# Kernel tuning notes

Hardware: AMD Instinct MI355X
Metric: run time of the kernel (lower is better)

Reference implementation:

```python
import jax, jax.numpy as jnp
import numpy as np

B, S, D = 4, 1568, 1024
H = 16
HD = D // H  # 64


def setup_inputs() -> dict:
    key = jax.random.key(0)
    ks = jax.random.split(key, 9)
    scale = 0.02
    return {
        "hidden_states": jax.random.normal(ks[0], (B, S, D), dtype=jnp.float32),
        "Wq": jax.random.normal(ks[1], (D, D), dtype=jnp.float32) * scale,
        "bq": jnp.zeros((D,), dtype=jnp.float32),
        "Wk": jax.random.normal(ks[2], (D, D), dtype=jnp.float32) * scale,
        "bk": jnp.zeros((D,), dtype=jnp.float32),
        "Wv": jax.random.normal(ks[3], (D, D), dtype=jnp.float32) * scale,
        "bv": jnp.zeros((D,), dtype=jnp.float32),
        "Wp": jax.random.normal(ks[4], (D, D), dtype=jnp.float32) * scale,
        "bp": jnp.zeros((D,), dtype=jnp.float32),
    }


def reference(hidden_states, Wq, bq, Wk, bk, Wv, bv, Wp, bp):
    x = hidden_states  # [B, S, D]
    # Linear projections (torch Linear: x @ W.T + b)
    q = x @ Wq.T + bq
    k = x @ Wk.T + bk
    v = x @ Wv.T + bv
    # split heads: [B, H, S, HD]
    def heads(t):
        return t.reshape(B, S, H, HD).transpose(0, 2, 1, 3)
    q, k, v = heads(q), heads(k), heads(v)
    scale = 1.0 / jnp.sqrt(jnp.asarray(HD, dtype=q.dtype))
    scores = jnp.einsum('bhqd,bhkd->bhqk', q, k) * scale  # [B,H,S,S]
    probs = jax.nn.softmax(scores, axis=-1)
    ctx = jnp.einsum('bhqk,bhkd->bhqd', probs, v)  # [B,H,S,HD]
    ctx = ctx.transpose(0, 2, 1, 3).reshape(B, S, D)
    out = ctx @ Wp.T + bp
    return out
```

## Files before the change

kernel.cpp:

```cpp
#include <hip/hip_runtime.h>
#include <stdint.h>

#define SEQ 1568
#define SEQV 1600
#define DIM 1024
#define NB 4
#define NH 16
#define HD 64

typedef unsigned short u16;
typedef __bf16 bf16x8 __attribute__((ext_vector_type(8)));
typedef float f32x4 __attribute__((ext_vector_type(4)));

#define QSCALE 0.18033688011112042f

#define PSTR 72

__device__ __forceinline__ void load_lds16(const u16* g, u16* s) {
  __builtin_amdgcn_global_load_lds((__attribute__((address_space(1))) void*)g,
                                   (__attribute__((address_space(3))) void*)s,
                                   16, 0, 0);
}

#define WAIT_VM(N) asm volatile("s_waitcnt vmcnt(" #N ")" ::: "memory")
#define LGKM0()    asm volatile("s_waitcnt lgkmcnt(0)" ::: "memory")
#define BAR()      do { __builtin_amdgcn_s_barrier(); \
                        __builtin_amdgcn_sched_barrier(0); } while (0)

__global__ __launch_bounds__(256) void cvt_all(
    const float* __restrict__ x,  const float* __restrict__ wq,
    const float* __restrict__ wk, const float* __restrict__ wv,
    const float* __restrict__ wp,
    u16* __restrict__ xb, u16* __restrict__ wqb, u16* __restrict__ wkb,
    u16* __restrict__ wvb, u16* __restrict__ wpb) {
  int i = blockIdx.x * 256 + threadIdx.x;
  const float* src; u16* dst; int off;
  if (i < 1605632)      { src = x;  dst = xb;  off = i; }
  else if (i < 1867776) { src = wq; dst = wqb; off = i - 1605632; }
  else if (i < 2129920) { src = wk; dst = wkb; off = i - 1867776; }
  else if (i < 2392064) { src = wv; dst = wvb; off = i - 2129920; }
  else                  { src = wp; dst = wpb; off = i - 2392064; }
  float4 v = ((const float4*)src)[off];
  union { unsigned long long u; __bf16 h[4]; } o;
  o.h[0] = (__bf16)v.x; o.h[1] = (__bf16)v.y;
  o.h[2] = (__bf16)v.z; o.h[3] = (__bf16)v.w;
  ((unsigned long long*)dst)[off] = o.u;
}

__global__ __launch_bounds__(256) void gemm_qkv(
    const u16* __restrict__ xb,
    const u16* __restrict__ wq, const u16* __restrict__ wk, const u16* __restrict__ wv,
    const float* __restrict__ bq, const float* __restrict__ bk, const float* __restrict__ bv,
    u16* __restrict__ qo, u16* __restrict__ ko, u16* __restrict__ vto) {
  const int bid = blockIdx.x + (blockIdx.y << 3) + blockIdx.z * 416;
  const int logical = (bid & 7) * 156 + (bid >> 3);
  const int byz = logical >> 3;
  const int by  = byz % 52;
  const int z   = byz / 52;
  const int bi  = by / 13;
  const int st  = by % 13;
  const int bn  = (logical & 7) * 128;

  const u16* W = (z == 0) ? wq : (z == 1) ? wk : wv;
  const float* bias = (z == 0) ? bq : (z == 1) ? bk : bv;

  __shared__ __align__(16) u16 sA[3][128 * 32];
  __shared__ __align__(16) u16 sB[3][128 * 32];

  const int tid = threadIdx.x;
  const int wave = tid >> 6;
  const int lane = tid & 63;
  const int l15 = lane & 15;
  const int quad = lane >> 4;
  const int wm = (wave >> 1) * 64;
  const int wn = (wave & 1) * 64;

  const int sr  = lane >> 2;
  const int scs = (((lane & 3) ^ ((lane >> 3) & 3)) << 3);
  const int r0 = wave * 32;

  int ra1 = st * 128 + r0 + sr;       if (ra1 >= SEQ) ra1 = SEQ - 1;
  int ra2 = st * 128 + r0 + 16 + sr;  if (ra2 >= SEQ) ra2 = SEQ - 1;
  const u16* gA1 = xb + (size_t)(bi * SEQ + ra1) * DIM + scs;
  const u16* gA2 = xb + (size_t)(bi * SEQ + ra2) * DIM + scs;
  const u16* gB1 = W + (size_t)(bn + r0 + sr) * DIM + scs;
  const u16* gB2 = gB1 + 16 * DIM;

  f32x4 acc[4][4] = {};
  const int rsw = (l15 >> 1) & 3;

  auto stage = [&](int kk, u16* sAc, u16* sBc) {
    load_lds16(gA1 + kk, sAc + r0 * 32);
    load_lds16(gA2 + kk, sAc + (r0 + 16) * 32);
    load_lds16(gB1 + kk, sBc + r0 * 32);
    load_lds16(gB2 + kk, sBc + (r0 + 16) * 32);
  };

  auto mstep = [&](const u16* sAc, const u16* sBc) {
    bf16x8 a[4], b[4];
#pragma unroll
    for (int mt = 0; mt < 4; mt++)
      a[mt] = *(const bf16x8*)&sAc[(wm + mt * 16 + l15) * 32 + ((quad ^ rsw) << 3)];
#pragma unroll
    for (int nt = 0; nt < 4; nt++)
      b[nt] = *(const bf16x8*)&sBc[(wn + nt * 16 + l15) * 32 + ((quad ^ rsw) << 3)];
#pragma unroll
    for (int mt = 0; mt < 4; mt++)
#pragma unroll
      for (int nt = 0; nt < 4; nt++)
        acc[mt][nt] = __builtin_amdgcn_mfma_f32_16x16x32_bf16(a[mt], b[nt], acc[mt][nt], 0, 0, 0);
  };

  stage(0,  &sA[0][0], &sB[0][0]);
  stage(32, &sA[1][0], &sB[1][0]);
  stage(64, &sA[2][0], &sB[2][0]);

#pragma unroll 1
  for (int t = 0; t < 30; t += 3) {
    WAIT_VM(8); BAR();
    mstep(&sA[0][0], &sB[0][0]);
    LGKM0(); BAR();
    stage((t + 3) * 32, &sA[0][0], &sB[0][0]);

    WAIT_VM(8); BAR();
    mstep(&sA[1][0], &sB[1][0]);
    LGKM0(); BAR();
    stage((t + 4) * 32, &sA[1][0], &sB[1][0]);

    WAIT_VM(8); BAR();
    mstep(&sA[2][0], &sB[2][0]);
    LGKM0(); BAR();
    if (t + 5 < 32) stage((t + 5) * 32, &sA[2][0], &sB[2][0]);
  }
  WAIT_VM(4); BAR();
  mstep(&sA[0][0], &sB[0][0]);
  WAIT_VM(0); BAR();
  mstep(&sA[1][0], &sB[1][0]);

#pragma unroll
  for (int nt = 0; nt < 4; nt++) {
    const int n = bn + wn + nt * 16 + l15;
    const float bia = bias[n];
    const int h = n >> 6, d = n & 63;
#pragma unroll
    for (int mt = 0; mt < 4; mt++) {
      const int sbase = st * 128 + wm + mt * 16 + quad * 4;
#pragma unroll
      for (int r = 0; r < 4; r++) {
        const int s = sbase + r;
        if (s < SEQ) {
          float val = acc[mt][nt][r] + bia;
          if (z == 0) val *= QSCALE;
          const __bf16 o = (__bf16)val;
          if (z == 0)
            *(__bf16*)&qo[(((size_t)(bi * NH + h)) * SEQ + s) * HD + d] = o;
          else if (z == 1)
            *(__bf16*)&ko[(((size_t)(bi * NH + h)) * SEQ + s) * HD + d] = o;
          else
            *(__bf16*)&vto[(((size_t)(bi * NH + h)) * HD + d) * SEQV + s] = o;
        }
      }
    }
  }
}

__global__ __launch_bounds__(256, 4) void attn(
    const u16* __restrict__ q, const u16* __restrict__ k,
    const u16* __restrict__ vt, u16* __restrict__ ctx) {
  const int bh = blockIdx.y;
  const int qt = blockIdx.x;
  const int tid = threadIdx.x;
  const int wave = tid >> 6, lane = tid & 63, l15 = lane & 15, quad = lane >> 4;

  __shared__ __align__(16) u16 sK[64 * 64];
  __shared__ __align__(16) u16 sV[64 * 64];
  __shared__ __align__(16) u16 sP[4][32 * PSTR];

  const u16* qh = q + (size_t)bh * (SEQ * HD);
  const u16* kh = k + (size_t)bh * (SEQ * HD);
  const u16* vh = vt + (size_t)bh * (HD * SEQV);

  bf16x8 aq[2][2];
#pragma unroll
  for (int mt = 0; mt < 2; mt++) {
    int qrow = qt * 128 + wave * 32 + mt * 16 + l15;
    int qr = qrow < SEQ ? qrow : SEQ - 1;
    aq[mt][0] = *(const bf16x8*)&qh[(size_t)qr * HD + quad * 8];
    aq[mt][1] = *(const bf16x8*)&qh[(size_t)qr * HD + 32 + quad * 8];
  }

  f32x4 o[2][4] = {};
  float lrow[2][4] = {};

  const int jrow = lane >> 3;
  const int cg = (lane & 7) ^ jrow;
  u16* sPw = sP[wave];
  const int j7 = l15 & 7;

  for (int j0 = 0; j0 < 1536; j0 += 64) {
    __syncthreads();
    load_lds16(&kh[(size_t)(j0 + wave * 16 + jrow) * HD + cg * 8], &sK[(wave * 16) * 64]);
    load_lds16(&kh[(size_t)(j0 + wave * 16 + 8 + jrow) * HD + cg * 8], &sK[(wave * 16 + 8) * 64]);
    load_lds16(&vh[(size_t)(wave * 16 + jrow) * SEQV + j0 + cg * 8], &sV[(wave * 16) * 64]);
    load_lds16(&vh[(size_t)(wave * 16 + 8 + jrow) * SEQV + j0 + cg * 8], &sV[(wave * 16 + 8) * 64]);
    __syncthreads();

#pragma unroll
    for (int mt = 0; mt < 2; mt++) {
      f32x4 s[4];
#pragma unroll
      for (int jt = 0; jt < 4; jt++) {
        const int j = jt * 16 + l15;
        bf16x8 b0 = *(const bf16x8*)&sK[j * 64 + ((quad ^ j7) * 8)];
        bf16x8 b1 = *(const bf16x8*)&sK[j * 64 + (((4 + quad) ^ j7) * 8)];
        f32x4 acc = {};
        acc = __builtin_amdgcn_mfma_f32_16x16x32_bf16(aq[mt][0], b0, acc, 0, 0, 0);
        acc = __builtin_amdgcn_mfma_f32_16x16x32_bf16(aq[mt][1], b1, acc, 0, 0, 0);
        s[jt] = acc;
      }
#pragma unroll
      for (int jt = 0; jt < 4; jt++)
#pragma unroll
        for (int r = 0; r < 4; r++) {
          float p = __builtin_exp2f(s[jt][r]);
          lrow[mt][r] += p;
          *(__bf16*)&sPw[(mt * 16 + quad * 4 + r) * PSTR + jt * 16 + l15] = (__bf16)p;
        }
    }

    asm volatile("s_waitcnt lgkmcnt(0)" ::: "memory");

#pragma unroll
    for (int kc = 0; kc < 2; kc++) {
      bf16x8 ap0 = *(const bf16x8*)&sPw[l15 * PSTR + kc * 32 + quad * 8];
      bf16x8 ap1 = *(const bf16x8*)&sPw[(16 + l15) * PSTR + kc * 32 + quad * 8];
#pragma unroll
      for (int dt = 0; dt < 4; dt++) {
        const int d7 = l15 & 7;
        bf16x8 bv = *(const bf16x8*)&sV[(dt * 16 + l15) * 64 + (((kc * 4 + quad) ^ d7) * 8)];
        o[0][dt] = __builtin_amdgcn_mfma_f32_16x16x32_bf16(ap0, bv, o[0][dt], 0, 0, 0);
        o[1][dt] = __builtin_amdgcn_mfma_f32_16x16x32_bf16(ap1, bv, o[1][dt], 0, 0, 0);
      }
    }
  }

  {
    const int j0 = 1536;
    __syncthreads();
    if (wave < 2) {
      load_lds16(&kh[(size_t)(j0 + wave * 16 + jrow) * HD + cg * 8], &sK[(wave * 16) * 64]);
      load_lds16(&kh[(size_t)(j0 + wave * 16 + 8 + jrow) * HD + cg * 8], &sK[(wave * 16 + 8) * 64]);
    }
    load_lds16(&vh[(size_t)(wave * 16 + jrow) * SEQV + j0 + cg * 8], &sV[(wave * 16) * 64]);
    load_lds16(&vh[(size_t)(wave * 16 + 8 + jrow) * SEQV + j0 + cg * 8], &sV[(wave * 16 + 8) * 64]);
    __syncthreads();

#pragma unroll
    for (int mt = 0; mt < 2; mt++) {
      f32x4 s[2];
#pragma unroll
      for (int jt = 0; jt < 2; jt++) {
        const int j = jt * 16 + l15;
        bf16x8 b0 = *(const bf16x8*)&sK[j * 64 + ((quad ^ j7) * 8)];
        bf16x8 b1 = *(const bf16x8*)&sK[j * 64 + (((4 + quad) ^ j7) * 8)];
        f32x4 acc = {};
        acc = __builtin_amdgcn_mfma_f32_16x16x32_bf16(aq[mt][0], b0, acc, 0, 0, 0);
        acc = __builtin_amdgcn_mfma_f32_16x16x32_bf16(aq[mt][1], b1, acc, 0, 0, 0);
        s[jt] = acc;
      }
#pragma unroll
      for (int jt = 0; jt < 2; jt++)
#pragma unroll
        for (int r = 0; r < 4; r++) {
          float p = __builtin_exp2f(s[jt][r]);
          lrow[mt][r] += p;
          *(__bf16*)&sPw[(mt * 16 + quad * 4 + r) * PSTR + jt * 16 + l15] = (__bf16)p;
        }
    }

    asm volatile("s_waitcnt lgkmcnt(0)" ::: "memory");

    {
      bf16x8 ap0 = *(const bf16x8*)&sPw[l15 * PSTR + quad * 8];
      bf16x8 ap1 = *(const bf16x8*)&sPw[(16 + l15) * PSTR + quad * 8];
#pragma unroll
      for (int dt = 0; dt < 4; dt++) {
        const int d7 = l15 & 7;
        bf16x8 bv = *(const bf16x8*)&sV[(dt * 16 + l15) * 64 + ((quad ^ d7) * 8)];
        o[0][dt] = __builtin_amdgcn_mfma_f32_16x16x32_bf16(ap0, bv, o[0][dt], 0, 0, 0);
        o[1][dt] = __builtin_amdgcn_mfma_f32_16x16x32_bf16(ap1, bv, o[1][dt], 0, 0, 0);
      }
    }
  }

  const int bi = bh >> 4, h = bh & 15;
#pragma unroll
  for (int mt = 0; mt < 2; mt++) {
#pragma unroll
    for (int r = 0; r < 4; r++) {
      float l = lrow[mt][r];
#pragma unroll
      for (int off = 8; off >= 1; off >>= 1) l += __shfl_xor(l, off, 16);
      const int srow = qt * 128 + wave * 32 + mt * 16 + quad * 4 + r;
      if (srow < SEQ) {
        const float inv = 1.0f / l;
#pragma unroll
        for (int dt = 0; dt < 4; dt++)
          *(__bf16*)&ctx[((size_t)(bi * SEQ + srow)) * DIM + h * HD + dt * 16 + l15] =
              (__bf16)(o[mt][dt][r] * inv);
      }
    }
  }
}

__global__ __launch_bounds__(256) void gemm_out(
    const u16* __restrict__ ctx, const u16* __restrict__ wp,
    const float* __restrict__ bp, float* __restrict__ out) {
  __shared__ __align__(16) u16 sA[128 * 32];
  __shared__ __align__(16) u16 sB[128 * 32];

  const int tid = threadIdx.x;
  const int wave = tid >> 6;
  const int lane = tid & 63;
  const int l15 = lane & 15;
  const int quad = lane >> 4;
  const int bm = blockIdx.y * 128;
  const int bn = blockIdx.x * 128;
  const int wm = (wave >> 1) * 64;
  const int wn = (wave & 1) * 64;
  const int sr = lane >> 2;
  const int sc = (lane & 3) * 8;
  const int r0 = wave * 32;

  f32x4 acc[4][4] = {};

  for (int k0 = 0; k0 < DIM; k0 += 32) {
    __syncthreads();
    {
      const u16* gA = ctx + (size_t)(bm + r0 + sr) * DIM + k0 + sc;
      load_lds16(gA, &sA[r0 * 32]);
      load_lds16(gA + 16 * DIM, &sA[(r0 + 16) * 32]);
      const u16* gB = wp + (size_t)(bn + r0 + sr) * DIM + k0 + sc;
      load_lds16(gB, &sB[r0 * 32]);
      load_lds16(gB + 16 * DIM, &sB[(r0 + 16) * 32]);
    }
    __syncthreads();

    bf16x8 a[4], b[4];
#pragma unroll
    for (int mt = 0; mt < 4; mt++)
      a[mt] = *(const bf16x8*)&sA[(wm + mt * 16 + l15) * 32 + quad * 8];
#pragma unroll
    for (int nt = 0; nt < 4; nt++)
      b[nt] = *(const bf16x8*)&sB[(wn + nt * 16 + l15) * 32 + quad * 8];
#pragma unroll
    for (int mt = 0; mt < 4; mt++)
#pragma unroll
      for (int nt = 0; nt < 4; nt++)
        acc[mt][nt] = __builtin_amdgcn_mfma_f32_16x16x32_bf16(a[mt], b[nt], acc[mt][nt], 0, 0, 0);
  }

#pragma unroll
  for (int nt = 0; nt < 4; nt++) {
    const int n = bn + wn + nt * 16 + l15;
    const float bia = bp[n];
#pragma unroll
    for (int mt = 0; mt < 4; mt++) {
      const int mbase = bm + wm + mt * 16 + quad * 4;
#pragma unroll
      for (int r = 0; r < 4; r++)
        out[(size_t)(mbase + r) * DIM + n] = acc[mt][nt][r] + bia;
    }
  }
}

extern "C" void kernel_launch(void* const* d_in, const int* in_sizes, int n_in,
                              void* d_out, int out_size, void* d_ws, size_t ws_size,
                              hipStream_t stream) {
  const float* x  = (const float*)d_in[0];
  const float* Wq = (const float*)d_in[1];
  const float* bq = (const float*)d_in[2];
  const float* Wk = (const float*)d_in[3];
  const float* bk = (const float*)d_in[4];
  const float* Wv = (const float*)d_in[5];
  const float* bv = (const float*)d_in[6];
  const float* Wp = (const float*)d_in[7];
  const float* bp = (const float*)d_in[8];
  float* out = (float*)d_out;

  char* ws = (char*)d_ws;
  u16* xb   = (u16*)(ws + 0);
  u16* wqb  = (u16*)(ws + 12845056);
  u16* wkb  = (u16*)(ws + 14942208);
  u16* wvb  = (u16*)(ws + 17039360);
  u16* wpb  = (u16*)(ws + 19136512);
  u16* qb   = (u16*)(ws + 21233664);
  u16* kb   = (u16*)(ws + 34078720);
  u16* vtb  = (u16*)(ws + 46923776);
  u16* ctxb = (u16*)(ws + 60030976);

  cvt_all<<<10368, 256, 0, stream>>>(x, Wq, Wk, Wv, Wp, xb, wqb, wkb, wvb, wpb);
  gemm_qkv<<<dim3(8, 52, 3), 256, 0, stream>>>(xb, wqb, wkb, wvb, bq, bk, bv, qb, kb, vtb);
  attn<<<dim3(13, 64), 256, 0, stream>>>(qb, kb, vtb, ctxb);
  gemm_out<<<dim3(8, 49), 256, 0, stream>>>(ctxb, wpb, bp, out);
}
```

Baseline: 295.6 us.

## Transpose S MFMA operands for packed P stores and remap attention blocks

The QK^T MFMA operands are swapped so each lane holds a score column per query row. Each lane can then pack four bf16 probabilities into one 8-byte LDS store instead of four scalar 2-byte stores, and keep a single running row sum per tile. The row-sum reduction becomes two cross-quad shuffles plus a broadcast. The grid is flattened to 1D with a remap that interleaves blocks by groups of 8 (likely to spread each head's K/V reuse across XCDs/L2), at the cost of a little integer div/mod per block.

Result: no change. 291.8 us (-1.3%).

```diff
diff --git a/kernel.cpp b/kernel.cpp
--- a/kernel.cpp
+++ b/kernel.cpp
@@ -10,6 +10,7 @@
 
 typedef unsigned short u16;
 typedef __bf16 bf16x8 __attribute__((ext_vector_type(8)));
+typedef __bf16 bf16x4 __attribute__((ext_vector_type(4)));
 typedef float f32x4 __attribute__((ext_vector_type(4)));
 
 #define QSCALE 0.18033688011112042f
@@ -167,8 +168,10 @@
 __global__ __launch_bounds__(256, 4) void attn(
     const u16* __restrict__ q, const u16* __restrict__ k,
     const u16* __restrict__ vt, u16* __restrict__ ctx) {
-  const int bh = blockIdx.y;
-  const int qt = blockIdx.x;
+  const int bid = blockIdx.x;
+  const int logical = (bid & 7) * 104 + (bid >> 3);
+  const int bh = logical / 13;
+  const int qt = logical % 13;
   const int tid = threadIdx.x;
   const int wave = tid >> 6, lane = tid & 63, l15 = lane & 15, quad = lane >> 4;
 
@@ -190,7 +193,7 @@
   }
 
   f32x4 o[2][4] = {};
-  float lrow[2][4] = {};
+  float lsum[2] = {0.0f, 0.0f};
 
   const int jrow = lane >> 3;
   const int cg = (lane & 7) ^ jrow;
@@ -214,21 +217,24 @@
         bf16x8 b0 = *(const bf16x8*)&sK[j * 64 + ((quad ^ j7) * 8)];
         bf16x8 b1 = *(const bf16x8*)&sK[j * 64 + (((4 + quad) ^ j7) * 8)];
         f32x4 acc = {};
-        acc = __builtin_amdgcn_mfma_f32_16x16x32_bf16(aq[mt][0], b0, acc, 0, 0, 0);
-        acc = __builtin_amdgcn_mfma_f32_16x16x32_bf16(aq[mt][1], b1, acc, 0, 0, 0);
+        acc = __builtin_amdgcn_mfma_f32_16x16x32_bf16(b0, aq[mt][0], acc, 0, 0, 0);
+        acc = __builtin_amdgcn_mfma_f32_16x16x32_bf16(b1, aq[mt][1], acc, 0, 0, 0);
         s[jt] = acc;
       }
 #pragma unroll
-      for (int jt = 0; jt < 4; jt++)
+      for (int jt = 0; jt < 4; jt++) {
+        bf16x4 pk;
 #pragma unroll
         for (int r = 0; r < 4; r++) {
           float p = __builtin_exp2f(s[jt][r]);
-          lrow[mt][r] += p;
-          *(__bf16*)&sPw[(mt * 16 + quad * 4 + r) * PSTR + jt * 16 + l15] = (__bf16)p;
+          lsum[mt] += p;
+          pk[r] = (__bf16)p;
         }
-    }
-
-    asm volatile("s_waitcnt lgkmcnt(0)" ::: "memory");
+        *(bf16x4*)&sPw[(mt * 16 + l15) * PSTR + jt * 16 + quad * 4] = pk;
+      }
+    }
+
+    LGKM0();
 
 #pragma unroll
     for (int kc = 0; kc < 2; kc++) {
@@ -264,21 +270,24 @@
         bf16x8 b0 = *(const bf16x8*)&sK[j * 64 + ((quad ^ j7) * 8)];
         bf16x8 b1 = *(const bf16x8*)&sK[j * 64 + (((4 + quad) ^ j7) * 8)];
         f32x4 acc = {};
-        acc = __builtin_amdgcn_mfma_f32_16x16x32_bf16(aq[mt][0], b0, acc, 0, 0, 0);
-        acc = __builtin_amdgcn_mfma_f32_16x16x32_bf16(aq[mt][1], b1, acc, 0, 0, 0);
+        acc = __builtin_amdgcn_mfma_f32_16x16x32_bf16(b0, aq[mt][0], acc, 0, 0, 0);
+        acc = __builtin_amdgcn_mfma_f32_16x16x32_bf16(b1, aq[mt][1], acc, 0, 0, 0);
         s[jt] = acc;
       }
 #pragma unroll
-      for (int jt = 0; jt < 2; jt++)
+      for (int jt = 0; jt < 2; jt++) {
+        bf16x4 pk;
 #pragma unroll
         for (int r = 0; r < 4; r++) {
           float p = __builtin_exp2f(s[jt][r]);
-          lrow[mt][r] += p;
-          *(__bf16*)&sPw[(mt * 16 + quad * 4 + r) * PSTR + jt * 16 + l15] = (__bf16)p;
+          lsum[mt] += p;
+          pk[r] = (__bf16)p;
         }
-    }
-
-    asm volatile("s_waitcnt lgkmcnt(0)" ::: "memory");
+        *(bf16x4*)&sPw[(mt * 16 + l15) * PSTR + jt * 16 + quad * 4] = pk;
+      }
+    }
+
+    LGKM0();
 
     {
       bf16x8 ap0 = *(const bf16x8*)&sPw[l15 * PSTR + quad * 8];
@@ -294,16 +303,23 @@
   }
 
   const int bi = bh >> 4, h = bh & 15;
+  float Lq[2][4];
 #pragma unroll
   for (int mt = 0; mt < 2; mt++) {
+    float l = lsum[mt];
+    l += __shfl_xor(l, 16);
+    l += __shfl_xor(l, 32);
+#pragma unroll
+    for (int r = 0; r < 4; r++)
+      Lq[mt][r] = __shfl(l, quad * 4 + r, 16);
+  }
+#pragma unroll
+  for (int mt = 0; mt < 2; mt++) {
 #pragma unroll
     for (int r = 0; r < 4; r++) {
-      float l = lrow[mt][r];
-#pragma unroll
-      for (int off = 8; off >= 1; off >>= 1) l += __shfl_xor(l, off, 16);
       const int srow = qt * 128 + wave * 32 + mt * 16 + quad * 4 + r;
       if (srow < SEQ) {
-        const float inv = 1.0f / l;
+        const float inv = 1.0f / Lq[mt][r];
 #pragma unroll
         for (int dt = 0; dt < 4; dt++)
           *(__bf16*)&ctx[((size_t)(bi * SEQ + srow)) * DIM + h * HD + dt * 16 + l15] =
@@ -401,6 +417,6 @@
 
   cvt_all<<<10368, 256, 0, stream>>>(x, Wq, Wk, Wv, Wp, xb, wqb, wkb, wvb, wpb);
   gemm_qkv<<<dim3(8, 52, 3), 256, 0, stream>>>(xb, wqb, wkb, wvb, bq, bk, bv, qb, kb, vtb);
-  attn<<<dim3(13, 64), 256, 0, stream>>>(qb, kb, vtb, ctxb);
+  attn<<<832, 256, 0, stream>>>(qb, kb, vtb, ctxb);
   gemm_out<<<dim3(8, 49), 256, 0, stream>>>(ctxb, wpb, bp, out);
 }
```
